# Optimization experiments

Measured on AMD Instinct MI355X. Metric: run time of the kernel, lower is better.

Reference implementation:

```python
import jax, jax.numpy as jnp
import numpy as np

N_NODES = 100000
N_FEAT = 128
HIDDEN = 32
HEADS = 4
N_CLASSES = 40
N_EDGES = 1600000
NEG_SLOPE = 0.2


def gat_conv(x, src, dst, W, att_src, att_dst, bias):
    """PyG-style GATConv (concat=True, eval mode, self-loops already in src/dst).
    x: [N, Fin], W: [Fin, H*C], att_src/att_dst: [H, C], bias: [H*C].
    """
    N = x.shape[0]
    H, C = att_src.shape
    h = (x @ W).reshape(N, H, C)                       # [N, H, C]
    a_src = jnp.einsum('nhc,hc->nh', h, att_src)       # [N, H]
    a_dst = jnp.einsum('nhc,hc->nh', h, att_dst)       # [N, H]
    e = a_src[src] + a_dst[dst]                        # [E, H]
    e = jnp.where(e > 0, e, NEG_SLOPE * e)             # leaky_relu(0.2)
    # segment softmax over incoming edges of each destination node
    e_max = jax.ops.segment_max(e, dst, num_segments=N)
    e = jnp.exp(e - e_max[dst])
    denom = jax.ops.segment_sum(e, dst, num_segments=N)
    alpha = e / (denom[dst] + 1e-16)                   # [E, H]
    msg = alpha[:, :, None] * h[src]                   # [E, H, C]
    out = jax.ops.segment_sum(msg, dst, num_segments=N)  # [N, H, C]
    return out.reshape(N, H * C) + bias


def setup_inputs() -> dict:
    key = jax.random.key(0)
    ks = jax.random.split(key, 10)
    s = 0.1
    x = jax.random.normal(ks[0], (N_NODES, N_FEAT), dtype=jnp.float32)
    edge_index = jax.random.randint(ks[1], (2, N_EDGES), 0, N_NODES, dtype=jnp.int32)
    W1 = jax.random.normal(ks[2], (N_FEAT, HEADS * HIDDEN), dtype=jnp.float32) * s
    att_src1 = jax.random.normal(ks[3], (HEADS, HIDDEN), dtype=jnp.float32) * s
    att_dst1 = jax.random.normal(ks[4], (HEADS, HIDDEN), dtype=jnp.float32) * s
    b1 = jnp.zeros((HEADS * HIDDEN,), dtype=jnp.float32)
    W2 = jax.random.normal(ks[5], (HEADS * HIDDEN, HEADS * HIDDEN), dtype=jnp.float32) * s
    att_src2 = jax.random.normal(ks[6], (HEADS, HIDDEN), dtype=jnp.float32) * s
    att_dst2 = jax.random.normal(ks[7], (HEADS, HIDDEN), dtype=jnp.float32) * s
    b2 = jnp.zeros((HEADS * HIDDEN,), dtype=jnp.float32)
    Wc = jax.random.normal(ks[8], (HEADS * HIDDEN, N_CLASSES), dtype=jnp.float32) * s
    bc = jnp.zeros((N_CLASSES,), dtype=jnp.float32)
    return {"x": x, "edge_index": edge_index, "W1": W1, "att_src1": att_src1,
            "att_dst1": att_dst1, "b1": b1, "W2": W2, "att_src2": att_src2,
            "att_dst2": att_dst2, "b2": b2, "Wc": Wc, "bc": bc}


def reference(x, edge_index, W1, att_src1, att_dst1, b1, W2, att_src2, att_dst2, b2, Wc, bc):
    N = x.shape[0]
    loops = jnp.arange(N, dtype=edge_index.dtype)
    src = jnp.concatenate([edge_index[0], loops])  # PyG add_self_loops=True
    dst = jnp.concatenate([edge_index[1], loops])
    h = gat_conv(x, src, dst, W1, att_src1, att_dst1, b1)
    h = jax.nn.relu(h)  # dropout p=0.5 inactive in eval
    h = gat_conv(h, src, dst, W2, att_src2, att_dst2, b2)
    h = jax.nn.relu(h)  # dropout p=0.6 inactive in eval
    return h @ Wc + bc
```

## Files before the change

kernel.cpp:

```cpp
#include <hip/hip_runtime.h>

#define NN    100000
#define NE    1600000
#define BSH   9
#define BSZ   512
#define NBK   196
#define TA    8192
#define NBA   196
#define CAP2R 8960
#define CAP2  9472
#define NBG   782
#define WPAD  136
#define RLN2  1.4426950408889634f

typedef _Float16 half_t;
typedef __attribute__((ext_vector_type(2))) _Float16 f16x2;
typedef __attribute__((ext_vector_type(4))) _Float16 f16x4;
typedef __attribute__((ext_vector_type(8))) _Float16 f16x8;
typedef __attribute__((ext_vector_type(4))) float    f32x4;

__device__ inline float fast_exp2(float x) {
#if __has_builtin(__builtin_amdgcn_exp2f)
  return __builtin_amdgcn_exp2f(x);
#else
  return exp2f(x);
#endif
}

__global__ __launch_bounds__(256) void k_prep(const float* __restrict__ W1, const float* __restrict__ W2,
                                              const float* __restrict__ Wc,
                                              const float* __restrict__ as1, const float* __restrict__ ad1,
                                              const float* __restrict__ as2, const float* __restrict__ ad2,
                                              half_t* __restrict__ WT1, half_t* __restrict__ WT2,
                                              half_t* __restrict__ WTc) {
  __shared__ float tile[64][65];
  int b = blockIdx.x, t = threadIdx.x;
  if (b < 10) {
    const float* W; half_t* WT; int k0, n0, N, NTr;
    if (b < 4)      { W = W1; WT = WT1; k0 = (b >> 1) * 64; n0 = (b & 1) * 64; N = 128; NTr = 128; }
    else if (b < 8) { int bb = b - 4; W = W2; WT = WT2; k0 = (bb >> 1) * 64; n0 = (bb & 1) * 64; N = 128; NTr = 128; }
    else            { int bb = b - 8; W = Wc; WT = WTc; k0 = bb * 64; n0 = 0; N = 40; NTr = 48; }
    int col = t & 63, r4 = t >> 6;
#pragma unroll
    for (int i = 0; i < 16; i++) {
      int row = r4 * 16 + i;
      float v = 0.f;
      if (n0 + col < N) v = W[(size_t)(k0 + row) * N + n0 + col];
      tile[row][col] = v;
    }
    __syncthreads();
#pragma unroll
    for (int i = 0; i < 16; i++) {
      int nrow = r4 * 16 + i;
      if (n0 + nrow < NTr) WT[(size_t)(n0 + nrow) * 128 + k0 + col] = (half_t)tile[col][nrow];
    }
    return;
  }
  const float* W  = (b == 10) ? W1 : W2;
  const float* as = (b == 10) ? as1 : as2;
  const float* ad = (b == 10) ? ad1 : ad2;
  half_t* WT      = (b == 10) ? WT1 : WT2;
  int e = t >> 5, kr = t & 31, h = e & 3;
  const float* att = ((e < 4) ? as : ad) + h * 32;
#pragma unroll
  for (int u = 0; u < 4; u++) {
    int k = u * 32 + kr;
    const float* wrow = W + (size_t)k * 128 + h * 32;
    float s = 0.f;
#pragma unroll
    for (int c = 0; c < 32; c += 4) {
      float4 wv = *(const float4*)(wrow + c);
      float4 av = *(const float4*)(att + c);
      s += wv.x * av.x + wv.y * av.y + wv.z * av.z + wv.w * av.w;
    }
    WT[(size_t)(128 + e) * 128 + k] = (half_t)(s * RLN2);
  }
  for (int u = t; u < 8 * 128; u += 256) WT[(size_t)136 * 128 + u] = (half_t)0.f;
}

__global__ __launch_bounds__(256) void k_front(const float* __restrict__ X, const half_t* __restrict__ WT1,
                                               half_t* __restrict__ H, float* __restrict__ asrc,
                                               float* __restrict__ adst,
                                               const int* __restrict__ src, const int* __restrict__ dst,
                                               unsigned int* __restrict__ bpk, int* __restrict__ gcnt) {
  __shared__ __align__(16) char smem[39168];
  int t = threadIdx.x;
  int bid = blockIdx.x;

  if (bid < NBA) {
    int hb = bid;
    int* hist  = (int*)smem;
    int* hscan = hist + NBK;
    int* cnt   = hscan + NBK;
    int* ssc   = cnt + NBK;
    unsigned int* staged = (unsigned int*)(ssc + 256);
    int e0 = hb * TA;
    if (t < NBK) { hist[t] = 0; cnt[t] = 0; }
    __syncthreads();
    for (int i = 0; i < TA / 256; i++) {
      int e = e0 + t + i * 256;
      if (e < NE) atomicAdd(&hist[dst[e] >> BSH], 1);
    }
    __syncthreads();
    {
      int v = (t < NBK) ? hist[t] : 0;
      int x = v;
      ssc[t] = x;
      for (int off = 1; off < 256; off <<= 1) {
        __syncthreads();
        int y = (t >= off) ? ssc[t - off] : 0;
        __syncthreads();
        x += y;
        ssc[t] = x;
      }
      if (t < NBK) hscan[t] = x - v;
    }
    __syncthreads();
    for (int i = 0; i < TA / 256; i++) {
      int e = e0 + t + i * 256;
      if (e < NE) {
        int d = dst[e];
        int bk = d >> BSH;
        int pos = hscan[bk] + atomicAdd(&cnt[bk], 1);
        staged[pos] = ((unsigned int)src[e] << BSH) | (unsigned int)(d & (BSZ - 1));
      }
    }
    __syncthreads();
    if (t < NBK) {
      int c = hist[t];
      cnt[t] = (c > 0) ? atomicAdd(&gcnt[t], c) : 0;
    }
    __syncthreads();
    int wave = t >> 6, lane = t & 63;
    for (int bk = wave; bk < NBK; bk += 4) {
      int c = hist[bk];
      int lo = hscan[bk];
      int base = cnt[bk];
      int avail = CAP2R - base;
      int cw = min(c, max(avail, 0));
      size_t bb = (size_t)bk * CAP2R + base;
      for (int j = lane; j < cw; j += 64) bpk[bb + j] = staged[lo + j];
    }
    return;
  }

  half_t* Wt = (half_t*)smem;
  int wave = t >> 6, lane = t & 63;
  int l15 = lane & 15, quad = lane >> 4;
  int rb = (bid - NBA) * 128;

  for (int c = t; c < 2304; c += 256) {
    int row = c >> 4;
    int c8 = (c & 15) * 8;
    *(f16x8*)(Wt + row * WPAD + c8) = *(const f16x8*)(WT1 + (size_t)row * 128 + c8);
  }
  __syncthreads();

  int rowA0 = rb + wave * 32 + l15;
  int rowA1 = rowA0 + 16;
  bool v0 = rowA0 < NN, v1 = rowA1 < NN;
  const float* xp0 = X + (size_t)rowA0 * 128 + quad * 8;
  const float* xp1 = X + (size_t)rowA1 * 128 + quad * 8;

  f32x4 acc[2][9];
#pragma unroll
  for (int rt = 0; rt < 2; rt++)
#pragma unroll
    for (int ct = 0; ct < 9; ct++) acc[rt][ct] = (f32x4){0.f, 0.f, 0.f, 0.f};

#pragma unroll
  for (int kk = 0; kk < 4; kk++) {
    int k0 = kk * 32;
    f16x8 a0 = (f16x8)(half_t)0, a1 = (f16x8)(half_t)0;
    if (v0) {
      float4 p = *(const float4*)(xp0 + k0);
      float4 q = *(const float4*)(xp0 + k0 + 4);
      a0[0] = (half_t)p.x; a0[1] = (half_t)p.y; a0[2] = (half_t)p.z; a0[3] = (half_t)p.w;
      a0[4] = (half_t)q.x; a0[5] = (half_t)q.y; a0[6] = (half_t)q.z; a0[7] = (half_t)q.w;
    }
    if (v1) {
      float4 p = *(const float4*)(xp1 + k0);
      float4 q = *(const float4*)(xp1 + k0 + 4);
      a1[0] = (half_t)p.x; a1[1] = (half_t)p.y; a1[2] = (half_t)p.z; a1[3] = (half_t)p.w;
      a1[4] = (half_t)q.x; a1[5] = (half_t)q.y; a1[6] = (half_t)q.z; a1[7] = (half_t)q.w;
    }
#pragma unroll
    for (int ct = 0; ct < 9; ct++) {
      f16x8 b = *(const f16x8*)(Wt + (ct * 16 + l15) * WPAD + k0 + quad * 8);
      acc[0][ct] = __builtin_amdgcn_mfma_f32_16x16x32_f16(a0, b, acc[0][ct], 0, 0, 0);
      acc[1][ct] = __builtin_amdgcn_mfma_f32_16x16x32_f16(a1, b, acc[1][ct], 0, 0, 0);
    }
  }

#pragma unroll
  for (int rt = 0; rt < 2; rt++) {
    int rbase = rb + wave * 32 + rt * 16 + quad * 4;
#pragma unroll
    for (int reg = 0; reg < 4; reg++) {
      int row = rbase + reg;
      if (row < NN) {
#pragma unroll
        for (int ct = 0; ct < 8; ct++) {
          H[(size_t)row * 128 + ct * 16 + l15] = (half_t)acc[rt][ct][reg];
        }
        if (l15 < 8) {
          float v = acc[rt][8][reg];
          if (l15 < 4) asrc[row * 4 + l15] = v;
          else         adst[row * 4 + (l15 - 4)] = v;
        }
      }
    }
  }
}

__global__ __launch_bounds__(512) void k_binB(const unsigned int* __restrict__ bpk,
                                              const int* __restrict__ gcnt,
                                              int* __restrict__ sbeg, int* __restrict__ send,
                                              int* __restrict__ adj) {
  __shared__ int lhist[BSZ];
  __shared__ int lscan[BSZ];
  __shared__ int lcur[BSZ];
  __shared__ int ssc[512];
  __shared__ unsigned int staged[CAP2];
  int b = blockIdx.x;
  int t = threadIdx.x;
  int nbeg = b << BSH;
  int nloc = min(BSZ, NN - nbeg);
  int adjb = b * CAP2;
  int cr = min(gcnt[b], CAP2R);
  size_t rbase = (size_t)b * CAP2R;
  lhist[t] = (t < nloc) ? 1 : 0;
  lcur[t] = 1;
  __syncthreads();
  for (int j = t; j < cr; j += 512) atomicAdd(&lhist[bpk[rbase + j] & (BSZ - 1)], 1);
  __syncthreads();
  {
    int v = lhist[t];
    int x = v;
    ssc[t] = x;
    for (int off = 1; off < 512; off <<= 1) {
      __syncthreads();
      int y = (t >= off) ? ssc[t - off] : 0;
      __syncthreads();
      x += y;
      ssc[t] = x;
    }
    lscan[t] = x - v;
  }
  __syncthreads();
  int total = lscan[BSZ - 1] + lhist[BSZ - 1];
  if (t < nloc) {
    int bg = adjb + lscan[t];
    sbeg[nbeg + t] = bg;
    send[nbeg + t] = bg + lhist[t];
    staged[lscan[t]] = (unsigned int)(nbeg + t);
  }
  __syncthreads();
  for (int j = t; j < cr; j += 512) {
    unsigned int v = bpk[rbase + j];
    int dl = v & (BSZ - 1);
    int idx = lscan[dl] + atomicAdd(&lcur[dl], 1);
    if (idx < CAP2) staged[idx] = v >> BSH;
  }
  __syncthreads();
  int lim = min(total, CAP2);
  for (int i = t; i < lim; i += 512) adj[adjb + i] = (int)staged[i];
}

__global__ __launch_bounds__(256) void k_agg(const half_t* __restrict__ H, const int* __restrict__ sbeg,
                                             const int* __restrict__ send, const int* __restrict__ adj,
                                             const float* __restrict__ asrc, const float* __restrict__ adst,
                                             const float* __restrict__ bias, half_t* __restrict__ out) {
  int n = blockIdx.x * 4 + (threadIdx.x >> 6);
  if (n >= NN) return;
  int lane = threadIdx.x & 63;
  int sub = lane & 7;
  int g = lane >> 3;
  int head = sub >> 1;
  float ad = adst[(size_t)n * 4 + head];
  float acc[16];
#pragma unroll
  for (int j = 0; j < 16; j++) acc[j] = 0.f;
  float wsum = 0.f;
  int beg = sbeg[n], end = send[n];
  int i = beg + g;
  int s = 0;
  float a = 0.f;
  f16x8 h0 = (f16x8)(half_t)0, h1 = (f16x8)(half_t)0;
  if (i < end) {
    s = adj[i];
    a = asrc[(size_t)s * 4 + head];
    const f16x8* hp = (const f16x8*)(H + (size_t)s * 128 + sub * 16);
    h0 = hp[0]; h1 = hp[1];
  }
  while (i < end) {
    int inext = i + 8;
    int sn = 0;
    float an = 0.f;
    if (inext < end) {
      sn = adj[inext];
      an = asrc[(size_t)sn * 4 + head];
    }
    const f16x8* hpn = (const f16x8*)(H + (size_t)sn * 128 + sub * 16);
    f16x8 g0 = hpn[0], g1 = hpn[1];
    float ev = a + ad;
    ev = (ev > 0.f) ? ev : 0.2f * ev;
    float w = fast_exp2(ev);
    wsum += w;
#pragma unroll
    for (int j = 0; j < 8; j++) acc[j] += w * (float)h0[j];
#pragma unroll
    for (int j = 0; j < 8; j++) acc[8 + j] += w * (float)h1[j];
    s = sn; a = an; h0 = g0; h1 = g1; i = inext;
  }
#pragma unroll
  for (int m = 8; m < 64; m <<= 1) {
    wsum += __shfl_xor(wsum, m, 64);
#pragma unroll
    for (int j = 0; j < 16; j++) acc[j] += __shfl_xor(acc[j], m, 64);
  }
  float scale = 1.0f / (wsum + 1e-16f);
  float o0 = acc[0], o1 = acc[1];
#pragma unroll
  for (int r = 1; r < 8; r++) {
    if (g == r) { o0 = acc[2 * r]; o1 = acc[2 * r + 1]; }
  }
  int ch = sub * 16 + g * 2;
  o0 = fmaxf(o0 * scale + bias[ch], 0.f);
  o1 = fmaxf(o1 * scale + bias[ch + 1], 0.f);
  f16x2 o;
  o[0] = (half_t)o0;
  o[1] = (half_t)o1;
  *(f16x2*)(out + (size_t)n * 128 + ch) = o;
}

__global__ __launch_bounds__(256) void k_gemm_att(const half_t* __restrict__ X, const half_t* __restrict__ WT,
                                                  half_t* __restrict__ H, float* __restrict__ asrc,
                                                  float* __restrict__ adst) {
  __shared__ __align__(16) half_t Wt[144 * WPAD];
  int t = threadIdx.x;
  int wave = t >> 6, lane = t & 63;
  int l15 = lane & 15, quad = lane >> 4;
  int rb = blockIdx.x * 64;

  for (int c = t; c < 2304; c += 256) {
    int row = c >> 4;
    int c8 = (c & 15) * 8;
    *(f16x8*)(Wt + row * WPAD + c8) = *(const f16x8*)(WT + (size_t)row * 128 + c8);
  }
  __syncthreads();

  int rowA = rb + wave * 16 + l15;
  bool va = rowA < NN;
  const half_t* xp = X + (size_t)rowA * 128 + quad * 8;

  f32x4 acc[9];
#pragma unroll
  for (int ct = 0; ct < 9; ct++) acc[ct] = (f32x4){0.f, 0.f, 0.f, 0.f};

#pragma unroll
  for (int kk = 0; kk < 4; kk++) {
    int k0 = kk * 32;
    f16x8 a0 = (f16x8)(half_t)0;
    if (va) a0 = *(const f16x8*)(xp + k0);
#pragma unroll
    for (int ct = 0; ct < 9; ct++) {
      f16x8 b = *(const f16x8*)(Wt + (ct * 16 + l15) * WPAD + k0 + quad * 8);
      acc[ct] = __builtin_amdgcn_mfma_f32_16x16x32_f16(a0, b, acc[ct], 0, 0, 0);
    }
  }

  int rbase = rb + wave * 16 + quad * 4;
#pragma unroll
  for (int reg = 0; reg < 4; reg++) {
    int row = rbase + reg;
    if (row < NN) {
#pragma unroll
      for (int ct = 0; ct < 8; ct++) {
        H[(size_t)row * 128 + ct * 16 + l15] = (half_t)acc[ct][reg];
      }
      if (l15 < 8) {
        float v = acc[8][reg];
        if (l15 < 4) asrc[row * 4 + l15] = v;
        else         adst[row * 4 + (l15 - 4)] = v;
      }
    }
  }
}

__global__ __launch_bounds__(256) void k_classifier(const half_t* __restrict__ Hf, const half_t* __restrict__ WTc,
                                                    const float* __restrict__ bc, float* __restrict__ out) {
  __shared__ __align__(16) half_t Wt[48 * WPAD];
  int t = threadIdx.x;
  int wave = t >> 6, lane = t & 63;
  int l15 = lane & 15, quad = lane >> 4;
  int rb = blockIdx.x * 64;

  for (int c = t; c < 768; c += 256) {
    int row = c >> 4;
    int c8 = (c & 15) * 8;
    *(f16x8*)(Wt + row * WPAD + c8) = *(const f16x8*)(WTc + (size_t)row * 128 + c8);
  }
  __syncthreads();

  int rowA = rb + wave * 16 + l15;
  bool va = rowA < NN;
  const half_t* xp = Hf + (size_t)rowA * 128 + quad * 8;

  f32x4 acc[3];
#pragma unroll
  for (int ct = 0; ct < 3; ct++) acc[ct] = (f32x4){0.f, 0.f, 0.f, 0.f};

#pragma unroll
  for (int kk = 0; kk < 4; kk++) {
    int k0 = kk * 32;
    f16x8 a0 = (f16x8)(half_t)0;
    if (va) a0 = *(const f16x8*)(xp + k0);
#pragma unroll
    for (int ct = 0; ct < 3; ct++) {
      f16x8 b = *(const f16x8*)(Wt + (ct * 16 + l15) * WPAD + k0 + quad * 8);
      acc[ct] = __builtin_amdgcn_mfma_f32_16x16x32_f16(a0, b, acc[ct], 0, 0, 0);
    }
  }

#pragma unroll
  for (int ct = 0; ct < 3; ct++) {
    int col = ct * 16 + l15;
    if (col < 40) {
      float bv = bc[col];
#pragma unroll
      for (int reg = 0; reg < 4; reg++) {
        int row = rb + wave * 16 + quad * 4 + reg;
        if (row < NN) out[(size_t)row * 40 + col] = acc[ct][reg] + bv;
      }
    }
  }
}


extern "C" void kernel_launch(void* const* d_in, const int* in_sizes, int n_in,
                              void* d_out, int out_size, void* d_ws, size_t ws_size,
                              hipStream_t stream) {
  const float* x   = (const float*)d_in[0];
  const int*   ei  = (const int*)d_in[1];
  const float* W1  = (const float*)d_in[2];
  const float* as1 = (const float*)d_in[3];
  const float* ad1 = (const float*)d_in[4];
  const float* b1  = (const float*)d_in[5];
  const float* W2  = (const float*)d_in[6];
  const float* as2 = (const float*)d_in[7];
  const float* ad2 = (const float*)d_in[8];
  const float* b2  = (const float*)d_in[9];
  const float* Wc  = (const float*)d_in[10];
  const float* bc  = (const float*)d_in[11];
  float* out = (float*)d_out;

  const int* esrc = ei;
  const int* edst = ei + NE;

  char* w = (char*)d_ws;
  auto alloc = [&](size_t bytes) {
    void* p = (void*)w;
    w += (bytes + 255) & ~(size_t)255;
    return p;
  };
  half_t* A   = (half_t*)alloc(sizeof(half_t) * (size_t)NN * 128);
  half_t* B   = (half_t*)alloc(sizeof(half_t) * (size_t)NN * 128);
  float* asrc = (float*)alloc(sizeof(float) * (size_t)NN * 4);
  float* adst = (float*)alloc(sizeof(float) * (size_t)NN * 4);
  int* sbeg   = (int*)alloc(sizeof(int) * NN);
  int* send   = (int*)alloc(sizeof(int) * NN);
  unsigned int* bpk = (unsigned int*)alloc(sizeof(unsigned int) * (size_t)NBK * CAP2R);
  int* gcnt   = (int*)alloc(sizeof(int) * NBK);
  int* adj    = (int*)alloc(sizeof(int) * (size_t)NBK * CAP2);
  half_t* WT1 = (half_t*)alloc(sizeof(half_t) * 144 * 128);
  half_t* WT2 = (half_t*)alloc(sizeof(half_t) * 144 * 128);
  half_t* WTc = (half_t*)alloc(sizeof(half_t) * 48 * 128);

  hipMemsetAsync(gcnt, 0, sizeof(int) * NBK, stream);

  k_prep<<<12, 256, 0, stream>>>(W1, W2, Wc, as1, ad1, as2, ad2, WT1, WT2, WTc);

  k_front<<<NBA + NBG, 256, 0, stream>>>(x, WT1, A, asrc, adst, esrc, edst, bpk, gcnt);

  k_binB<<<NBK, 512, 0, stream>>>(bpk, gcnt, sbeg, send, adj);

  k_agg<<<(NN + 3) / 4, 256, 0, stream>>>(A, sbeg, send, adj, asrc, adst, b1, B);

  k_gemm_att<<<(NN + 63) / 64, 256, 0, stream>>>(B, WT2, A, asrc, adst);
  k_agg<<<(NN + 3) / 4, 256, 0, stream>>>(A, sbeg, send, adj, asrc, adst, b2, B);

  k_classifier<<<(NN + 63) / 64, 256, 0, stream>>>(B, WTc, bc, out);
}
```

Baseline: 354.3 us.

## Regroup front kernels: fuse binning with weight prep, CSR build with GEMM1

Reorganises the three front kernels into two launches. Edge binning now shares a launch with the weight transpose and attention folding, and the per-bucket CSR construction shares a launch with the first-layer GEMM. The CSR part moves from 512 to 256 threads, with each thread handling two histogram slots. This removes one kernel launch and lets the latency-bound CSR build overlap with the GEMM. The cost is higher shared-memory use per block in the fused kernel, which may lower occupancy for the GEMM blocks.

```diff
diff --git a/kernel.cpp b/kernel.cpp
--- a/kernel.cpp
+++ b/kernel.cpp
@@ -27,63 +27,15 @@
 #endif
 }
 
-__global__ __launch_bounds__(256) void k_prep(const float* __restrict__ W1, const float* __restrict__ W2,
-                                              const float* __restrict__ Wc,
-                                              const float* __restrict__ as1, const float* __restrict__ ad1,
-                                              const float* __restrict__ as2, const float* __restrict__ ad2,
-                                              half_t* __restrict__ WT1, half_t* __restrict__ WT2,
-                                              half_t* __restrict__ WTc) {
-  __shared__ float tile[64][65];
-  int b = blockIdx.x, t = threadIdx.x;
-  if (b < 10) {
-    const float* W; half_t* WT; int k0, n0, N, NTr;
-    if (b < 4)      { W = W1; WT = WT1; k0 = (b >> 1) * 64; n0 = (b & 1) * 64; N = 128; NTr = 128; }
-    else if (b < 8) { int bb = b - 4; W = W2; WT = WT2; k0 = (bb >> 1) * 64; n0 = (bb & 1) * 64; N = 128; NTr = 128; }
-    else            { int bb = b - 8; W = Wc; WT = WTc; k0 = bb * 64; n0 = 0; N = 40; NTr = 48; }
-    int col = t & 63, r4 = t >> 6;
-#pragma unroll
-    for (int i = 0; i < 16; i++) {
-      int row = r4 * 16 + i;
-      float v = 0.f;
-      if (n0 + col < N) v = W[(size_t)(k0 + row) * N + n0 + col];
-      tile[row][col] = v;
-    }
-    __syncthreads();
-#pragma unroll
-    for (int i = 0; i < 16; i++) {
-      int nrow = r4 * 16 + i;
-      if (n0 + nrow < NTr) WT[(size_t)(n0 + nrow) * 128 + k0 + col] = (half_t)tile[col][nrow];
-    }
-    return;
-  }
-  const float* W  = (b == 10) ? W1 : W2;
-  const float* as = (b == 10) ? as1 : as2;
-  const float* ad = (b == 10) ? ad1 : ad2;
-  half_t* WT      = (b == 10) ? WT1 : WT2;
-  int e = t >> 5, kr = t & 31, h = e & 3;
-  const float* att = ((e < 4) ? as : ad) + h * 32;
-#pragma unroll
-  for (int u = 0; u < 4; u++) {
-    int k = u * 32 + kr;
-    const float* wrow = W + (size_t)k * 128 + h * 32;
-    float s = 0.f;
-#pragma unroll
-    for (int c = 0; c < 32; c += 4) {
-      float4 wv = *(const float4*)(wrow + c);
-      float4 av = *(const float4*)(att + c);
-      s += wv.x * av.x + wv.y * av.y + wv.z * av.z + wv.w * av.w;
-    }
-    WT[(size_t)(128 + e) * 128 + k] = (half_t)(s * RLN2);
-  }
-  for (int u = t; u < 8 * 128; u += 256) WT[(size_t)136 * 128 + u] = (half_t)0.f;
-}
-
-__global__ __launch_bounds__(256) void k_front(const float* __restrict__ X, const half_t* __restrict__ WT1,
-                                               half_t* __restrict__ H, float* __restrict__ asrc,
-                                               float* __restrict__ adst,
-                                               const int* __restrict__ src, const int* __restrict__ dst,
-                                               unsigned int* __restrict__ bpk, int* __restrict__ gcnt) {
-  __shared__ __align__(16) char smem[39168];
+__global__ __launch_bounds__(256) void k1_bin_prep(const int* __restrict__ src, const int* __restrict__ dst,
+                                                   unsigned int* __restrict__ bpk, int* __restrict__ gcnt,
+                                                   const float* __restrict__ W1, const float* __restrict__ W2,
+                                                   const float* __restrict__ Wc,
+                                                   const float* __restrict__ as1, const float* __restrict__ ad1,
+                                                   const float* __restrict__ as2, const float* __restrict__ ad2,
+                                                   half_t* __restrict__ WT1, half_t* __restrict__ WT2,
+                                                   half_t* __restrict__ WTc) {
+  __shared__ __align__(16) char smem[36864];
   int t = threadIdx.x;
   int bid = blockIdx.x;
 
@@ -144,10 +96,126 @@
     return;
   }
 
+  int b = bid - NBA;
+  if (b < 10) {
+    float (*tile)[65] = (float(*)[65])smem;
+    const float* W; half_t* WT; int k0, n0, N, NTr;
+    if (b < 4)      { W = W1; WT = WT1; k0 = (b >> 1) * 64; n0 = (b & 1) * 64; N = 128; NTr = 128; }
+    else if (b < 8) { int bb = b - 4; W = W2; WT = WT2; k0 = (bb >> 1) * 64; n0 = (bb & 1) * 64; N = 128; NTr = 128; }
+    else            { int bb = b - 8; W = Wc; WT = WTc; k0 = bb * 64; n0 = 0; N = 40; NTr = 48; }
+    int col = t & 63, r4 = t >> 6;
+#pragma unroll
+    for (int i = 0; i < 16; i++) {
+      int row = r4 * 16 + i;
+      float v = 0.f;
+      if (n0 + col < N) v = W[(size_t)(k0 + row) * N + n0 + col];
+      tile[row][col] = v;
+    }
+    __syncthreads();
+#pragma unroll
+    for (int i = 0; i < 16; i++) {
+      int nrow = r4 * 16 + i;
+      if (n0 + nrow < NTr) WT[(size_t)(n0 + nrow) * 128 + k0 + col] = (half_t)tile[col][nrow];
+    }
+    return;
+  }
+  const float* W  = (b == 10) ? W1 : W2;
+  const float* as = (b == 10) ? as1 : as2;
+  const float* ad = (b == 10) ? ad1 : ad2;
+  half_t* WT      = (b == 10) ? WT1 : WT2;
+  int e = t >> 5, kr = t & 31, h = e & 3;
+  const float* att = ((e < 4) ? as : ad) + h * 32;
+#pragma unroll
+  for (int u = 0; u < 4; u++) {
+    int k = u * 32 + kr;
+    const float* wrow = W + (size_t)k * 128 + h * 32;
+    float s = 0.f;
+#pragma unroll
+    for (int c = 0; c < 32; c += 4) {
+      float4 wv = *(const float4*)(wrow + c);
+      float4 av = *(const float4*)(att + c);
+      s += wv.x * av.x + wv.y * av.y + wv.z * av.z + wv.w * av.w;
+    }
+    WT[(size_t)(128 + e) * 128 + k] = (half_t)(s * RLN2);
+  }
+  for (int u = t; u < 8 * 128; u += 256) WT[(size_t)136 * 128 + u] = (half_t)0.f;
+}
+
+__global__ __launch_bounds__(256) void k2_csr_gemm1(const unsigned int* __restrict__ bpk,
+                                                    const int* __restrict__ gcnt,
+                                                    int* __restrict__ sbeg, int* __restrict__ send,
+                                                    int* __restrict__ adj,
+                                                    const float* __restrict__ X, const half_t* __restrict__ WT1,
+                                                    half_t* __restrict__ H, float* __restrict__ asrc,
+                                                    float* __restrict__ adst) {
+  __shared__ __align__(16) char smem[45056];
+  int t = threadIdx.x;
+  int bid = blockIdx.x;
+
+  if (bid < NBK) {
+    int* lhist = (int*)smem;
+    int* lscan = lhist + BSZ;
+    int* lcur  = lscan + BSZ;
+    int* ssc   = lcur + BSZ;
+    unsigned int* staged = (unsigned int*)(ssc + 256);
+    int b = bid;
+    int nbeg = b << BSH;
+    int nloc = min(BSZ, NN - nbeg);
+    int adjb = b * CAP2;
+    int cr = min(gcnt[b], CAP2R);
+    size_t rbase = (size_t)b * CAP2R;
+    lhist[2 * t] = (2 * t < nloc) ? 1 : 0;
+    lhist[2 * t + 1] = (2 * t + 1 < nloc) ? 1 : 0;
+    lcur[2 * t] = 1;
+    lcur[2 * t + 1] = 1;
+    __syncthreads();
+    for (int j = t; j < cr; j += 256) atomicAdd(&lhist[bpk[rbase + j] & (BSZ - 1)], 1);
+    __syncthreads();
+    {
+      int v0 = lhist[2 * t], v1 = lhist[2 * t + 1];
+      int s2 = v0 + v1;
+      int x = s2;
+      ssc[t] = x;
+      for (int off = 1; off < 256; off <<= 1) {
+        __syncthreads();
+        int y = (t >= off) ? ssc[t - off] : 0;
+        __syncthreads();
+        x += y;
+        ssc[t] = x;
+      }
+      int ex = x - s2;
+      lscan[2 * t] = ex;
+      lscan[2 * t + 1] = ex + v0;
+    }
+    __syncthreads();
+    int total = lscan[BSZ - 1] + lhist[BSZ - 1];
+#pragma unroll
+    for (int u = 0; u < 2; u++) {
+      int i2 = t + u * 256;
+      if (i2 < nloc) {
+        int bg = adjb + lscan[i2];
+        sbeg[nbeg + i2] = bg;
+        send[nbeg + i2] = bg + lhist[i2];
+        staged[lscan[i2]] = (unsigned int)(nbeg + i2);
+      }
+    }
+    __syncthreads();
+    for (int j = t; j < cr; j += 256) {
+      unsigned int v = bpk[rbase + j];
+      int dl = v & (BSZ - 1);
+      int idx = lscan[dl] + atomicAdd(&lcur[dl], 1);
+      if (idx < CAP2) staged[idx] = v >> BSH;
+    }
+    __syncthreads();
+    int lim = min(total, CAP2);
+    for (int i2 = t; i2 < lim; i2 += 256) adj[adjb + i2] = (int)staged[i2];
+    return;
+  }
+
   half_t* Wt = (half_t*)smem;
   int wave = t >> 6, lane = t & 63;
   int l15 = lane & 15, quad = lane >> 4;
-  int rb = (bid - NBA) * 128;
+  int rb = (bid - NBK) * 128;
 
   for (int c = t; c < 2304; c += 256) {
     int row = c >> 4;
@@ -211,60 +279,6 @@
       }
     }
   }
-}
-
-__global__ __launch_bounds__(512) void k_binB(const unsigned int* __restrict__ bpk,
-                                              const int* __restrict__ gcnt,
-                                              int* __restrict__ sbeg, int* __restrict__ send,
-                                              int* __restrict__ adj) {
-  __shared__ int lhist[BSZ];
-  __shared__ int lscan[BSZ];
-  __shared__ int lcur[BSZ];
-  __shared__ int ssc[512];
-  __shared__ unsigned int staged[CAP2];
-  int b = blockIdx.x;
-  int t = threadIdx.x;
-  int nbeg = b << BSH;
-  int nloc = min(BSZ, NN - nbeg);
-  int adjb = b * CAP2;
-  int cr = min(gcnt[b], CAP2R);
-  size_t rbase = (size_t)b * CAP2R;
-  lhist[t] = (t < nloc) ? 1 : 0;
-  lcur[t] = 1;
-  __syncthreads();
-  for (int j = t; j < cr; j += 512) atomicAdd(&lhist[bpk[rbase + j] & (BSZ - 1)], 1);
-  __syncthreads();
-  {
-    int v = lhist[t];
-    int x = v;
-    ssc[t] = x;
-    for (int off = 1; off < 512; off <<= 1) {
-      __syncthreads();
-      int y = (t >= off) ? ssc[t - off] : 0;
-      __syncthreads();
-      x += y;
-      ssc[t] = x;
-    }
-    lscan[t] = x - v;
-  }
-  __syncthreads();
-  int total = lscan[BSZ - 1] + lhist[BSZ - 1];
-  if (t < nloc) {
-    int bg = adjb + lscan[t];
-    sbeg[nbeg + t] = bg;
-    send[nbeg + t] = bg + lhist[t];
-    staged[lscan[t]] = (unsigned int)(nbeg + t);
-  }
-  __syncthreads();
-  for (int j = t; j < cr; j += 512) {
-    unsigned int v = bpk[rbase + j];
-    int dl = v & (BSZ - 1);
-    int idx = lscan[dl] + atomicAdd(&lcur[dl], 1);
-    if (idx < CAP2) staged[idx] = v >> BSH;
-  }
-  __syncthreads();
-  int lim = min(total, CAP2);
-  for (int i = t; i < lim; i += 512) adj[adjb + i] = (int)staged[i];
 }
 
 __global__ __launch_bounds__(256) void k_agg(const half_t* __restrict__ H, const int* __restrict__ sbeg,
@@ -479,11 +493,11 @@
 
   hipMemsetAsync(gcnt, 0, sizeof(int) * NBK, stream);
 
-  k_prep<<<12, 256, 0, stream>>>(W1, W2, Wc, as1, ad1, as2, ad2, WT1, WT2, WTc);
-
-  k_front<<<NBA + NBG, 256, 0, stream>>>(x, WT1, A, asrc, adst, esrc, edst, bpk, gcnt);
-
-  k_binB<<<NBK, 512, 0, stream>>>(bpk, gcnt, sbeg, send, adj);
+  k1_bin_prep<<<NBA + 12, 256, 0, stream>>>(esrc, edst, bpk, gcnt,
+                                            W1, W2, Wc, as1, ad1, as2, ad2, WT1, WT2, WTc);
+
+  k2_csr_gemm1<<<NBK + NBG, 256, 0, stream>>>(bpk, gcnt, sbeg, send, adj,
+                                              x, WT1, A, asrc, adst);
 
   k_agg<<<(NN + 3) / 4, 256, 0, stream>>>(A, sbeg, send, adj, asrc, adst, b1, B);
 
```

After: 346.9 us. 1.02x faster.
